# Performance work log

Measured on AMD Instinct MI355X. Metric: run time of the kernel, lower is better.

## Reference

```python
import jax, jax.numpy as jnp
import numpy as np

B, T, D = 64, 512, 512
H, DH = 8, 64  # head_num, att_embedding_size; H*DH == D
NEG = jnp.float32(-2.0**32 + 1)


def _pos_encoding(t, d):
    # Position_Embedding (mode='sum'): [cos, sin] concat over d/2 frequencies
    inv_freq = 1.0 / jnp.power(10000.0, 2.0 * jnp.arange(d // 2, dtype=jnp.float32) / d)
    pij = jnp.arange(t, dtype=jnp.float32)[:, None] * inv_freq[None, :]  # (T, d/2)
    return jnp.concatenate([jnp.cos(pij), jnp.sin(pij)], axis=-1)  # (T, d)


def setup_inputs() -> dict:
    key = jax.random.key(0)
    ks = jax.random.split(key, 9)
    queries = jax.random.normal(ks[0], (B, T, D), dtype=jnp.float32)
    keys = jax.random.normal(ks[1], (B, T, D), dtype=jnp.float32)
    query_lens = jax.random.randint(ks[2], (B, 1), 1, T + 1)
    key_lens = jax.random.randint(ks[3], (B, 1), 1, T + 1)
    W_Q = jax.random.truncated_normal(ks[4], -2., 2., (D, H * DH), dtype=jnp.float32) * 0.05
    W_K = jax.random.truncated_normal(ks[5], -2., 2., (D, H * DH), dtype=jnp.float32) * 0.05
    W_V = jax.random.truncated_normal(ks[6], -2., 2., (D, H * DH), dtype=jnp.float32) * 0.05
    fw1 = jax.random.normal(ks[7], (H * DH, 4 * H * DH), dtype=jnp.float32) * 0.02
    fw2 = jax.random.normal(ks[8], (4 * H * DH, H * DH), dtype=jnp.float32) * 0.02
    return {"queries": queries, "keys": keys, "query_lens": query_lens,
            "key_lens": key_lens, "W_Q": W_Q, "W_K": W_K, "W_V": W_V,
            "fw1": fw1, "fw2": fw2}


def reference(queries, keys, query_lens, key_lens, W_Q, W_K, W_V, fw1, fw2):
    # sequence masks (B, T) from lengths (B, 1)
    ar = jnp.arange(T)
    q_mask = (ar[None, :] < query_lens).astype(jnp.float32)  # (B, T)
    k_mask = ar[None, :] < key_lens                          # (B, T) bool

    pe = _pos_encoding(T, D)[None]  # (1, T, D)
    q_in = queries + pe
    k_in = keys + pe

    qp = jnp.einsum('btd,de->bte', q_in, W_Q).reshape(B, T, H, DH)
    kp = jnp.einsum('btd,de->bte', k_in, W_K)
    # DeepCTR quirk: values projected from the already-projected keys
    vp = jnp.einsum('btd,de->bte', kp, W_V).reshape(B, T, H, DH)
    kp = kp.reshape(B, T, H, DH)

    scores = jnp.einsum('bthd,bshd->bhts', qp, kp) / jnp.sqrt(jnp.float32(DH))
    scores = jnp.where(k_mask[:, None, None, :], scores, NEG)
    scores = scores - jnp.max(scores, axis=-1, keepdims=True)
    attn = jax.nn.softmax(scores, axis=-1)
    attn = attn * q_mask[:, None, :, None]

    out = jnp.einsum('bhts,bshd->bthd', attn, vp).reshape(B, T, H * DH)
    result = out + q_in  # residual uses PE-augmented queries

    ff = jnp.einsum('btd,df->btf', jax.nn.relu(jnp.einsum('btd,df->btf', result, fw1)), fw2)
    result = result + ff

    return jnp.mean(result, axis=1, keepdims=True)  # (B, 1, D)
```

## Files before the change

kernel.cpp:

```cpp
#include <hip/hip_runtime.h>

typedef unsigned short u16;
typedef __attribute__((ext_vector_type(8))) short short8;
typedef __attribute__((ext_vector_type(4))) float floatx4;

#define LOG2E 1.44269504f

__device__ __forceinline__ u16 f2bf(float x) {
  union { float f; unsigned u; } un; un.f = x;
  unsigned r = un.u + 0x7fffu + ((un.u >> 16) & 1u);
  return (u16)(r >> 16);
}
__device__ __forceinline__ float bf2f(u16 h) {
  union { unsigned u; float f; } un; un.u = ((unsigned)h) << 16;
  return un.f;
}
__device__ __forceinline__ void gld16(const u16* g, u16* l) {
  __builtin_amdgcn_global_load_lds((__attribute__((address_space(1))) void*)g,
                                   (__attribute__((address_space(3))) void*)l, 16, 0, 0);
}

__global__ __launch_bounds__(256) void wtrans_kernel(const float* __restrict__ in,
                                                     u16* __restrict__ out, int K, int N) {
  __shared__ float tile[32][33];
  int tx = threadIdx.x, ty = threadIdx.y;
  int n0 = blockIdx.x * 32, k0 = blockIdx.y * 32;
#pragma unroll
  for (int i = 0; i < 4; i++) {
    int kk = ty + i * 8;
    tile[kk][tx] = in[(size_t)(k0 + kk) * N + n0 + tx];
  }
  __syncthreads();
#pragma unroll
  for (int i = 0; i < 4; i++) {
    int nn = ty + i * 8;
    out[(size_t)(n0 + nn) * K + k0 + tx] = f2bf(tile[tx][nn]);
  }
}

__global__ __launch_bounds__(256) void pe_add_kernel(const float* __restrict__ q,
                                                     const float* __restrict__ k,
                                                     u16* __restrict__ qb, u16* __restrict__ kb) {
  size_t flat = ((size_t)blockIdx.x * 256 + threadIdx.x) * 4;
  int d0 = (int)(flat & 511);
  int t = (int)((flat >> 9) & 511);
  const float4 qv = *(const float4*)(q + flat);
  const float4 kv = *(const float4*)(k + flat);
  float pe[4];
#pragma unroll
  for (int i = 0; i < 4; i++) {
    int d = d0 + i;
    int j = (d < 256) ? d : d - 256;
    float f = exp2f((float)j * -0.05190512648f);
    float arg = (float)t * f;
    pe[i] = (d < 256) ? cosf(arg) : sinf(arg);
  }
  u16 qo[4], ko[4];
  qo[0] = f2bf(qv.x + pe[0]); qo[1] = f2bf(qv.y + pe[1]);
  qo[2] = f2bf(qv.z + pe[2]); qo[3] = f2bf(qv.w + pe[3]);
  ko[0] = f2bf(kv.x + pe[0]); ko[1] = f2bf(kv.y + pe[1]);
  ko[2] = f2bf(kv.z + pe[2]); ko[3] = f2bf(kv.w + pe[3]);
  *(uint2*)(qb + flat) = *(const uint2*)qo;
  *(uint2*)(kb + flat) = *(const uint2*)ko;
}

template <int EPI, int DUAL>
__global__ __launch_bounds__(256) void gemm_bt(const u16* __restrict__ A, const u16* __restrict__ Bt,
                                               u16* __restrict__ C, int NX, int KS, int N, int K,
                                               float* __restrict__ outp,
                                               const u16* __restrict__ A2, const u16* __restrict__ Bt2,
                                               u16* __restrict__ C2) {
  __shared__ u16 Alds[128 * 64];
  __shared__ u16 Blds[128 * 64];
  const int tid = threadIdx.x;
  const int lane = tid & 63, w = tid >> 6;
  const int quad = lane >> 4, cl = lane & 15;
  const int wm = w >> 1, wn = w & 1;
  int L = blockIdx.x;
  if (DUAL) {
    int half = gridDim.x >> 1;
    if (L >= half) { L -= half; A = A2; Bt = Bt2; C = C2; }
  }
  const int xcd = L & 7, s = L >> 3;
  const int nx = s % NX;
  const int t2 = s / NX;
  const int ksl = t2 % KS;
  const int rgrp = t2 / KS;
  const int tm = (rgrp * 8 + xcd) * 128;
  const int tn = nx * 128;
  const int kbase = ksl * (K / KS);
  floatx4 acc[4][4] = {};
  const int nk = (K / KS) >> 6;
  const int srow = lane >> 3;
  const int sg = (lane & 7) ^ srow;
  for (int ks = 0; ks < nk; ks++) {
    __syncthreads();
    const int k0 = kbase + (ks << 6);
#pragma unroll
    for (int i = 0; i < 4; i++) {
      int c = w * 4 + i;
      int row = c * 8 + srow;
      gld16(A + ((size_t)(tm + row) * K + k0 + sg * 8), &Alds[c * 512]);
      gld16(Bt + ((size_t)(tn + row) * K + k0 + sg * 8), &Blds[c * 512]);
    }
    __syncthreads();
#pragma unroll
    for (int kh = 0; kh < 2; kh++) {
      short8 af[4], bfr[4];
      const int ga = (((kh << 2) + quad) ^ (cl & 7)) * 8;
#pragma unroll
      for (int f = 0; f < 4; f++) {
        af[f] = *(const short8*)&Alds[(wm * 64 + f * 16 + cl) * 64 + ga];
        bfr[f] = *(const short8*)&Blds[(wn * 64 + f * 16 + cl) * 64 + ga];
      }
#pragma unroll
      for (int fm = 0; fm < 4; fm++)
#pragma unroll
        for (int fn = 0; fn < 4; fn++)
          acc[fm][fn] = __builtin_amdgcn_mfma_f32_16x16x32_bf16(af[fm], bfr[fn], acc[fm][fn], 0, 0, 0);
    }
  }
  if constexpr (EPI == 0) {
#pragma unroll
    for (int fm = 0; fm < 4; fm++)
#pragma unroll
      for (int fn = 0; fn < 4; fn++)
#pragma unroll
        for (int r = 0; r < 4; r++) {
          int row = tm + wm * 64 + fm * 16 + quad * 4 + r;
          int col = tn + wn * 64 + fn * 16 + cl;
          C[(size_t)row * N + col] = f2bf(acc[fm][fn][r]);
        }
  } else if constexpr (EPI == 2) {
    __shared__ float red[256];
    float csum[4] = {0.f, 0.f, 0.f, 0.f};
#pragma unroll
    for (int fm = 0; fm < 4; fm++)
#pragma unroll
      for (int fn = 0; fn < 4; fn++)
#pragma unroll
        for (int r = 0; r < 4; r++) csum[fn] += fmaxf(acc[fm][fn][r], 0.0f);
#pragma unroll
    for (int fn = 0; fn < 4; fn++) {
      csum[fn] += __shfl_xor(csum[fn], 16);
      csum[fn] += __shfl_xor(csum[fn], 32);
    }
    __syncthreads();
    if (quad == 0) {
#pragma unroll
      for (int fn = 0; fn < 4; fn++) red[wm * 128 + wn * 64 + fn * 16 + cl] = csum[fn];
    }
    __syncthreads();
    if (tid < 128) {
      int wn2 = tid >> 6, c2 = tid & 63;
      float tot = red[wn2 * 64 + c2] + red[128 + wn2 * 64 + c2];
      int b = tm >> 9;
      atomicAdd(outp + (size_t)b * N + tn + wn2 * 64 + c2, tot);
    }
  } else {
    __shared__ u16 Tr[128][130];
#pragma unroll
    for (int fm = 0; fm < 4; fm++)
#pragma unroll
      for (int fn = 0; fn < 4; fn++)
#pragma unroll
        for (int r = 0; r < 4; r++) {
          int row = wm * 64 + fm * 16 + quad * 4 + r;
          int col = wn * 64 + fn * 16 + cl;
          Tr[col][row] = f2bf(acc[fm][fn][r]);
        }
    __syncthreads();
    int col = tid >> 1, half = tid & 1;
    int b = tm >> 9, gcol = tn + col;
    int h = gcol >> 6, d = gcol & 63;
    int s0 = (tm & 511) + half * 64;
    u16* dst = C + ((size_t)((b * 8 + h) * 64 + d) * 512 + s0);
    const u16* src = &Tr[col][half * 64];
#pragma unroll
    for (int j = 0; j < 8; j++) *(short8*)(dst + j * 8) = *(const short8*)(src + j * 8);
  }
}

__global__ __launch_bounds__(256) void ffn2_mean_kernel(const float* __restrict__ sums,
                                                        const float* __restrict__ fw2,
                                                        float* __restrict__ outp) {
  __shared__ float s[128];
  int fs = blockIdx.x & 15, b = blockIdx.x >> 4;
  int tid = threadIdx.x;
  if (tid < 128) s[tid] = sums[(size_t)b * 2048 + fs * 128 + tid];
  __syncthreads();
  const float* w = fw2 + (size_t)(fs * 128) * 512;
  float a0 = 0.f, a1 = 0.f;
#pragma unroll 4
  for (int f = 0; f < 128; f++) {
    float sv = s[f];
    a0 += sv * w[(size_t)f * 512 + tid];
    a1 += sv * w[(size_t)f * 512 + 256 + tid];
  }
  atomicAdd(outp + b * 512 + tid, a0 * (1.0f / 512.0f));
  atomicAdd(outp + b * 512 + 256 + tid, a1 * (1.0f / 512.0f));
}

__global__ __launch_bounds__(256) void attn_kernel(const u16* __restrict__ qp, const u16* __restrict__ kp,
                                                   const u16* __restrict__ vT, const u16* __restrict__ qin,
                                                   u16* __restrict__ resout, const int* __restrict__ qlen,
                                                   const int* __restrict__ klen, float* __restrict__ outp) {
  __shared__ u16 Klds[128 * 64];
  __shared__ u16 Vlds[64 * 128];
  __shared__ u16 Plds[4][16 * 136];
  __shared__ float Csum[4][64];
  int bid = blockIdx.x;
  int qt = bid & 7, h = (bid >> 3) & 7, b = bid >> 6;
  int tid = threadIdx.x, lane = tid & 63, w = tid >> 6;
  int quad = lane >> 4, cl = lane & 15;
  int kl = klen[b], ql = qlen[b];
  int q0 = qt * 64 + w * 16;

  if (qt * 64 >= ql) {
    int c = tid & 63, r0 = (tid >> 6) * 16;
    float s = 0.f;
#pragma unroll
    for (int i = 0; i < 16; i++) {
      size_t idx = ((size_t)(b * 512 + qt * 64 + r0 + i) * 512) + h * 64 + c;
      u16 val = qin[idx];
      resout[idx] = val;
      s += bf2f(val);
    }
    Csum[w][c] = s;
    __syncthreads();
    if (tid < 64) {
      float t = Csum[0][tid] + Csum[1][tid] + Csum[2][tid] + Csum[3][tid];
      atomicAdd(outp + b * 512 + h * 64 + tid, t * (1.0f / 512.0f));
    }
    return;
  }
  bool wactive = q0 < ql;

  short8 qfrag[2];
#pragma unroll
  for (int ks = 0; ks < 2; ks++)
    qfrag[ks] = *(const short8*)(qp + ((size_t)(b * 512 + q0 + cl) * 512 + h * 64 + ks * 32 + quad * 8));
  float m_r[4], l_r[4];
  floatx4 o[4] = {};
#pragma unroll
  for (int r = 0; r < 4; r++) { m_r[r] = -3.0e38f; l_r[r] = 0.f; }

  int nkt = (kl + 127) >> 7;
  for (int kt = 0; kt < nkt; kt++) {
    __syncthreads();
#pragma unroll
    for (int i = 0; i < 4; i++) {
      int c = w * 4 + i;
      int row = c * 8 + (lane >> 3);
      int gc = (lane & 7) ^ (row & 7);
      gld16(kp + ((size_t)(b * 512 + kt * 128 + row) * 512 + h * 64 + gc * 8), &Klds[c * 512]);
    }
#pragma unroll
    for (int i = 0; i < 4; i++) {
      int c = w * 4 + i;
      int row = c * 4 + (lane >> 4);
      int gc = (lane & 15) ^ (row & 7);
      gld16(vT + ((size_t)((b * 8 + h) * 64 + row) * 512 + kt * 128 + gc * 8), &Vlds[c * 512]);
    }
    __syncthreads();
    if (!wactive) continue;
    floatx4 sacc[8] = {};
#pragma unroll
    for (int f = 0; f < 8; f++) {
      int krow = f * 16 + cl;
#pragma unroll
      for (int ks = 0; ks < 2; ks++) {
        int kc = ks * 4 + quad;
        short8 kf = *(const short8*)&Klds[krow * 64 + ((kc ^ (cl & 7)) * 8)];
        sacc[f] = __builtin_amdgcn_mfma_f32_16x16x32_bf16(qfrag[ks], kf, sacc[f], 0, 0, 0);
      }
    }
    float mnew[4];
#pragma unroll
    for (int r = 0; r < 4; r++) mnew[r] = m_r[r];
#pragma unroll
    for (int f = 0; f < 8; f++) {
      int key = kt * 128 + f * 16 + cl;
      bool ok = key < kl;
#pragma unroll
      for (int r = 0; r < 4; r++) {
        float v = ok ? sacc[f][r] * 0.125f : -4294967296.0f;
        sacc[f][r] = v;
        mnew[r] = fmaxf(mnew[r], v);
      }
    }
#pragma unroll
    for (int mk = 1; mk <= 8; mk <<= 1)
#pragma unroll
      for (int r = 0; r < 4; r++) mnew[r] = fmaxf(mnew[r], __shfl_xor(mnew[r], mk));
    float alpha[4], lad[4];
#pragma unroll
    for (int r = 0; r < 4; r++) {
      alpha[r] = exp2f((m_r[r] - mnew[r]) * LOG2E);
      lad[r] = 0.f;
      m_r[r] = mnew[r];
    }
#pragma unroll
    for (int f = 0; f < 8; f++)
#pragma unroll
      for (int r = 0; r < 4; r++) {
        float p = exp2f((sacc[f][r] - mnew[r]) * LOG2E);
        lad[r] += p;
        Plds[w][(quad * 4 + r) * 136 + f * 16 + cl] = f2bf(p);
      }
#pragma unroll
    for (int mk = 1; mk <= 8; mk <<= 1)
#pragma unroll
      for (int r = 0; r < 4; r++) lad[r] += __shfl_xor(lad[r], mk);
#pragma unroll
    for (int r = 0; r < 4; r++) l_r[r] = l_r[r] * alpha[r] + lad[r];
#pragma unroll
    for (int fd = 0; fd < 4; fd++)
#pragma unroll
      for (int r = 0; r < 4; r++) o[fd][r] *= alpha[r];
#pragma unroll
    for (int k2 = 0; k2 < 4; k2++) {
      short8 pf = *(const short8*)&Plds[w][cl * 136 + k2 * 32 + quad * 8];
#pragma unroll
      for (int fd = 0; fd < 4; fd++) {
        int vrow = fd * 16 + cl;
        int sc = k2 * 4 + quad;
        short8 vf = *(const short8*)&Vlds[vrow * 128 + ((sc ^ (cl & 7)) * 8)];
        o[fd] = __builtin_amdgcn_mfma_f32_16x16x32_bf16(pf, vf, o[fd], 0, 0, 0);
      }
    }
  }
  float colsum[4] = {0.f, 0.f, 0.f, 0.f};
#pragma unroll
  for (int fd = 0; fd < 4; fd++)
#pragma unroll
    for (int r = 0; r < 4; r++) {
      int q = q0 + quad * 4 + r;
      float v = o[fd][r] / l_r[r];
      if (q >= ql) v = 0.f;
      size_t idx = (size_t)(b * 512 + q) * 512 + h * 64 + fd * 16 + cl;
      v += bf2f(qin[idx]);
      resout[idx] = f2bf(v);
      colsum[fd] += v;
    }
#pragma unroll
  for (int fd = 0; fd < 4; fd++) {
    colsum[fd] += __shfl_xor(colsum[fd], 16);
    colsum[fd] += __shfl_xor(colsum[fd], 32);
  }
  if (quad == 0) {
#pragma unroll
    for (int fd = 0; fd < 4; fd++) Csum[w][fd * 16 + cl] = colsum[fd];
  }
  __syncthreads();
  if (tid < 64) {
    float t = Csum[0][tid] + Csum[1][tid] + Csum[2][tid] + Csum[3][tid];
    atomicAdd(outp + b * 512 + h * 64 + tid, t * (1.0f / 512.0f));
  }
}

extern "C" void kernel_launch(void* const* d_in, const int* in_sizes, int n_in,
                              void* d_out, int out_size, void* d_ws, size_t ws_size,
                              hipStream_t stream) {
  const float* queries = (const float*)d_in[0];
  const float* keys = (const float*)d_in[1];
  const int* qlen = (const int*)d_in[2];
  const int* klen = (const int*)d_in[3];
  const float* W_Q = (const float*)d_in[4];
  const float* W_K = (const float*)d_in[5];
  const float* W_V = (const float*)d_in[6];
  const float* fw1 = (const float*)d_in[7];
  const float* fw2 = (const float*)d_in[8];
  float* outp = (float*)d_out;
  char* ws = (char*)d_ws;

  constexpr size_t SZ_W = 512 * 512 * 2;
  constexpr size_t SZ_F = 2048 * 512 * 2;
  constexpr size_t SZ_S = 64 * 2048 * 4;
  constexpr size_t SZ_T = (size_t)64 * 512 * 512 * 2;
  size_t o_WqT = 0;
  size_t o_WkT = o_WqT + SZ_W;
  size_t o_WvT = o_WkT + SZ_W;
  size_t o_F1T = o_WvT + SZ_W;
  size_t o_SUM = o_F1T + SZ_F;
  size_t o_ABCD = o_SUM + SZ_S;
  size_t o_E = o_ABCD + 4 * SZ_T;
  size_t NEED = o_E + SZ_T;
  if (ws_size < NEED) return;

  u16* WqT = (u16*)(ws + o_WqT);
  u16* WkT = (u16*)(ws + o_WkT);
  u16* WvT = (u16*)(ws + o_WvT);
  u16* F1T = (u16*)(ws + o_F1T);
  float* sums = (float*)(ws + o_SUM);
  u16* q_in = (u16*)(ws + o_ABCD);
  u16* k_in = (u16*)(ws + o_ABCD + SZ_T);
  u16* qp = (u16*)(ws + o_ABCD + 2 * SZ_T);
  u16* kpb = (u16*)(ws + o_ABCD + 3 * SZ_T);
  u16* vT = k_in;
  u16* resb = (u16*)(ws + o_E);

  hipMemsetAsync(d_out, 0, (size_t)out_size * sizeof(float), stream);
  hipMemsetAsync(sums, 0, SZ_S, stream);

  dim3 tb(32, 8);
  wtrans_kernel<<<dim3(16, 16), tb, 0, stream>>>(W_Q, WqT, 512, 512);
  wtrans_kernel<<<dim3(16, 16), tb, 0, stream>>>(W_K, WkT, 512, 512);
  wtrans_kernel<<<dim3(16, 16), tb, 0, stream>>>(W_V, WvT, 512, 512);
  wtrans_kernel<<<dim3(64, 16), tb, 0, stream>>>(fw1, F1T, 512, 2048);

  pe_add_kernel<<<16384, 256, 0, stream>>>(queries, keys, q_in, k_in);

  gemm_bt<0, 1><<<2 * 4 * 256, 256, 0, stream>>>(q_in, WqT, qp, 4, 1, 512, 512, nullptr, k_in, WkT, kpb);
  gemm_bt<3, 0><<<4 * 256, 256, 0, stream>>>(kpb, WvT, vT, 4, 1, 512, 512, nullptr, nullptr, nullptr, nullptr);

  attn_kernel<<<4096, 256, 0, stream>>>(qp, kpb, vT, q_in, resb, qlen, klen, outp);

  gemm_bt<2, 0><<<16 * 256, 256, 0, stream>>>(resb, F1T, nullptr, 16, 1, 2048, 512, sums, nullptr, nullptr, nullptr);
  ffn2_mean_kernel<<<1024, 256, 0, stream>>>(sums, fw2, outp);
}
```

Before: 423.9 us.

## Stage full per-head K/V in LDS once and loop all query tiles per block

Measured after the change: 459.4 us. 8.4% more time.

```diff
diff --git a/kernel.cpp b/kernel.cpp
--- a/kernel.cpp
+++ b/kernel.cpp
@@ -205,144 +205,149 @@
                                                    const u16* __restrict__ vT, const u16* __restrict__ qin,
                                                    u16* __restrict__ resout, const int* __restrict__ qlen,
                                                    const int* __restrict__ klen, float* __restrict__ outp) {
-  __shared__ u16 Klds[128 * 64];
-  __shared__ u16 Vlds[64 * 128];
+  __shared__ u16 Klds[4 * 128 * 64];
+  __shared__ u16 Vlds[4 * 64 * 128];
   __shared__ u16 Plds[4][16 * 136];
-  __shared__ float Csum[4][64];
-  int bid = blockIdx.x;
-  int qt = bid & 7, h = (bid >> 3) & 7, b = bid >> 6;
-  int tid = threadIdx.x, lane = tid & 63, w = tid >> 6;
-  int quad = lane >> 4, cl = lane & 15;
-  int kl = klen[b], ql = qlen[b];
-  int q0 = qt * 64 + w * 16;
-
-  if (qt * 64 >= ql) {
-    int c = tid & 63, r0 = (tid >> 6) * 16;
-    float s = 0.f;
-#pragma unroll
-    for (int i = 0; i < 16; i++) {
-      size_t idx = ((size_t)(b * 512 + qt * 64 + r0 + i) * 512) + h * 64 + c;
-      u16 val = qin[idx];
-      resout[idx] = val;
-      s += bf2f(val);
-    }
-    Csum[w][c] = s;
-    __syncthreads();
-    if (tid < 64) {
-      float t = Csum[0][tid] + Csum[1][tid] + Csum[2][tid] + Csum[3][tid];
-      atomicAdd(outp + b * 512 + h * 64 + tid, t * (1.0f / 512.0f));
-    }
-    return;
-  }
-  bool wactive = q0 < ql;
-
-  short8 qfrag[2];
-#pragma unroll
-  for (int ks = 0; ks < 2; ks++)
-    qfrag[ks] = *(const short8*)(qp + ((size_t)(b * 512 + q0 + cl) * 512 + h * 64 + ks * 32 + quad * 8));
-  float m_r[4], l_r[4];
-  floatx4 o[4] = {};
-#pragma unroll
-  for (int r = 0; r < 4; r++) { m_r[r] = -3.0e38f; l_r[r] = 0.f; }
-
-  int nkt = (kl + 127) >> 7;
-  for (int kt = 0; kt < nkt; kt++) {
-    __syncthreads();
-#pragma unroll
-    for (int i = 0; i < 4; i++) {
-      int c = w * 4 + i;
-      int row = c * 8 + (lane >> 3);
-      int gc = (lane & 7) ^ (row & 7);
-      gld16(kp + ((size_t)(b * 512 + kt * 128 + row) * 512 + h * 64 + gc * 8), &Klds[c * 512]);
-    }
-#pragma unroll
-    for (int i = 0; i < 4; i++) {
-      int c = w * 4 + i;
-      int row = c * 4 + (lane >> 4);
+  const int bid = blockIdx.x;
+  const int h = bid & 7, b = bid >> 3;
+  const int tid = threadIdx.x, lane = tid & 63, w = tid >> 6;
+  const int quad = lane >> 4, cl = lane & 15;
+  const int kl = klen[b], ql = qlen[b];
+  const int nkt = (kl + 127) >> 7;
+
+  {
+    const int srow = lane >> 3;
+    const int sg = (lane & 7) ^ srow;
+    for (int c = w; c < nkt * 16; c += 4) {
+      int row = (c >> 4) * 128 + (c & 15) * 8 + srow;
+      gld16(kp + ((size_t)(b * 512 + row) * 512 + h * 64 + sg * 8), &Klds[c * 512]);
+    }
+    const int vr = lane >> 4;
+    for (int c = w; c < nkt * 16; c += 4) {
+      int row = (c & 15) * 4 + vr;
       int gc = (lane & 15) ^ (row & 7);
-      gld16(vT + ((size_t)((b * 8 + h) * 64 + row) * 512 + kt * 128 + gc * 8), &Vlds[c * 512]);
-    }
-    __syncthreads();
-    if (!wactive) continue;
-    floatx4 sacc[8] = {};
-#pragma unroll
-    for (int f = 0; f < 8; f++) {
-      int krow = f * 16 + cl;
-#pragma unroll
-      for (int ks = 0; ks < 2; ks++) {
-        int kc = ks * 4 + quad;
-        short8 kf = *(const short8*)&Klds[krow * 64 + ((kc ^ (cl & 7)) * 8)];
-        sacc[f] = __builtin_amdgcn_mfma_f32_16x16x32_bf16(qfrag[ks], kf, sacc[f], 0, 0, 0);
-      }
-    }
-    float mnew[4];
-#pragma unroll
-    for (int r = 0; r < 4; r++) mnew[r] = m_r[r];
-#pragma unroll
-    for (int f = 0; f < 8; f++) {
-      int key = kt * 128 + f * 16 + cl;
-      bool ok = key < kl;
+      gld16(vT + ((size_t)((b * 8 + h) * 64 + row) * 512 + (c >> 4) * 128 + gc * 8), &Vlds[c * 512]);
+    }
+  }
+
+  float colsum[4] = {0.f, 0.f, 0.f, 0.f};
+
+#pragma unroll 1
+  for (int p = 0; p < 8; p++) {
+    int q0 = p * 64 + w * 16;
+    if (q0 < ql) continue;
+#pragma unroll
+    for (int fd = 0; fd < 4; fd++)
 #pragma unroll
       for (int r = 0; r < 4; r++) {
-        float v = ok ? sacc[f][r] * 0.125f : -4294967296.0f;
-        sacc[f][r] = v;
-        mnew[r] = fmaxf(mnew[r], v);
-      }
-    }
-#pragma unroll
-    for (int mk = 1; mk <= 8; mk <<= 1)
-#pragma unroll
-      for (int r = 0; r < 4; r++) mnew[r] = fmaxf(mnew[r], __shfl_xor(mnew[r], mk));
-    float alpha[4], lad[4];
-#pragma unroll
-    for (int r = 0; r < 4; r++) {
-      alpha[r] = exp2f((m_r[r] - mnew[r]) * LOG2E);
-      lad[r] = 0.f;
-      m_r[r] = mnew[r];
-    }
-#pragma unroll
-    for (int f = 0; f < 8; f++)
+        int q = q0 + quad * 4 + r;
+        size_t idx = ((size_t)(b * 512 + q) * 512) + h * 64 + fd * 16 + cl;
+        u16 val = qin[idx];
+        resout[idx] = val;
+        colsum[fd] += bf2f(val);
+      }
+  }
+
+  __syncthreads();
+
+#pragma unroll 1
+  for (int p = 0; p < 8; p++) {
+    int q0 = p * 64 + w * 16;
+    if (q0 >= ql) continue;
+    short8 qfrag[2];
+#pragma unroll
+    for (int ks = 0; ks < 2; ks++)
+      qfrag[ks] = *(const short8*)(qp + ((size_t)(b * 512 + q0 + cl) * 512 + h * 64 + ks * 32 + quad * 8));
+    float m_r[4], l_r[4];
+    floatx4 o[4] = {};
+#pragma unroll
+    for (int r = 0; r < 4; r++) { m_r[r] = -3.0e38f; l_r[r] = 0.f; }
+
+#pragma unroll 1
+    for (int kt = 0; kt < nkt; kt++) {
+      const u16* Kt = &Klds[kt * 8192];
+      const u16* Vt = &Vlds[kt * 8192];
+      floatx4 sacc[8] = {};
+#pragma unroll
+      for (int f = 0; f < 8; f++) {
+        int krow = f * 16 + cl;
+#pragma unroll
+        for (int ks = 0; ks < 2; ks++) {
+          int kc = ks * 4 + quad;
+          short8 kf = *(const short8*)&Kt[krow * 64 + ((kc ^ (cl & 7)) * 8)];
+          sacc[f] = __builtin_amdgcn_mfma_f32_16x16x32_bf16(qfrag[ks], kf, sacc[f], 0, 0, 0);
+        }
+      }
+      float mnew[4];
+#pragma unroll
+      for (int r = 0; r < 4; r++) mnew[r] = m_r[r];
+#pragma unroll
+      for (int f = 0; f < 8; f++) {
+        int key = kt * 128 + f * 16 + cl;
+        bool ok = key < kl;
+#pragma unroll
+        for (int r = 0; r < 4; r++) {
+          float v = ok ? sacc[f][r] * 0.125f : -4294967296.0f;
+          sacc[f][r] = v;
+          mnew[r] = fmaxf(mnew[r], v);
+        }
+      }
+#pragma unroll
+      for (int mk = 1; mk <= 8; mk <<= 1)
+#pragma unroll
+        for (int r = 0; r < 4; r++) mnew[r] = fmaxf(mnew[r], __shfl_xor(mnew[r], mk));
+      float alpha[4], lad[4];
 #pragma unroll
       for (int r = 0; r < 4; r++) {
-        float p = exp2f((sacc[f][r] - mnew[r]) * LOG2E);
-        lad[r] += p;
-        Plds[w][(quad * 4 + r) * 136 + f * 16 + cl] = f2bf(p);
-      }
-#pragma unroll
-    for (int mk = 1; mk <= 8; mk <<= 1)
-#pragma unroll
-      for (int r = 0; r < 4; r++) lad[r] += __shfl_xor(lad[r], mk);
-#pragma unroll
-    for (int r = 0; r < 4; r++) l_r[r] = l_r[r] * alpha[r] + lad[r];
+        alpha[r] = exp2f((m_r[r] - mnew[r]) * LOG2E);
+        lad[r] = 0.f;
+        m_r[r] = mnew[r];
+      }
+#pragma unroll
+      for (int f = 0; f < 8; f++)
+#pragma unroll
+        for (int r = 0; r < 4; r++) {
+          float pv = exp2f((sacc[f][r] - mnew[r]) * LOG2E);
+          lad[r] += pv;
+          Plds[w][(quad * 4 + r) * 136 + f * 16 + cl] = f2bf(pv);
+        }
+#pragma unroll
+      for (int mk = 1; mk <= 8; mk <<= 1)
+#pragma unroll
+        for (int r = 0; r < 4; r++) lad[r] += __shfl_xor(lad[r], mk);
+#pragma unroll
+      for (int r = 0; r < 4; r++) l_r[r] = l_r[r] * alpha[r] + lad[r];
+#pragma unroll
+      for (int fd = 0; fd < 4; fd++)
+#pragma unroll
+        for (int r = 0; r < 4; r++) o[fd][r] *= alpha[r];
+#pragma unroll
+      for (int k2 = 0; k2 < 4; k2++) {
+        short8 pf = *(const short8*)&Plds[w][cl * 136 + k2 * 32 + quad * 8];
+#pragma unroll
+        for (int fd = 0; fd < 4; fd++) {
+          int vrow = fd * 16 + cl;
+          int sc = k2 * 4 + quad;
+          short8 vf = *(const short8*)&Vt[vrow * 128 + ((sc ^ (cl & 7)) * 8)];
+          o[fd] = __builtin_amdgcn_mfma_f32_16x16x32_bf16(pf, vf, o[fd], 0, 0, 0);
+        }
+      }
+    }
+
 #pragma unroll
     for (int fd = 0; fd < 4; fd++)
 #pragma unroll
-      for (int r = 0; r < 4; r++) o[fd][r] *= alpha[r];
-#pragma unroll
-    for (int k2 = 0; k2 < 4; k2++) {
-      short8 pf = *(const short8*)&Plds[w][cl * 136 + k2 * 32 + quad * 8];
-#pragma unroll
-      for (int fd = 0; fd < 4; fd++) {
-        int vrow = fd * 16 + cl;
-        int sc = k2 * 4 + quad;
-        short8 vf = *(const short8*)&Vlds[vrow * 128 + ((sc ^ (cl & 7)) * 8)];
-        o[fd] = __builtin_amdgcn_mfma_f32_16x16x32_bf16(pf, vf, o[fd], 0, 0, 0);
-      }
-    }
-  }
-  float colsum[4] = {0.f, 0.f, 0.f, 0.f};
-#pragma unroll
-  for (int fd = 0; fd < 4; fd++)
-#pragma unroll
-    for (int r = 0; r < 4; r++) {
-      int q = q0 + quad * 4 + r;
-      float v = o[fd][r] / l_r[r];
-      if (q >= ql) v = 0.f;
-      size_t idx = (size_t)(b * 512 + q) * 512 + h * 64 + fd * 16 + cl;
-      v += bf2f(qin[idx]);
-      resout[idx] = f2bf(v);
-      colsum[fd] += v;
-    }
+      for (int r = 0; r < 4; r++) {
+        int q = q0 + quad * 4 + r;
+        float v = o[fd][r] / l_r[r];
+        if (q >= ql) v = 0.f;
+        size_t idx = (size_t)(b * 512 + q) * 512 + h * 64 + fd * 16 + cl;
+        v += bf2f(qin[idx]);
+        resout[idx] = f2bf(v);
+        colsum[fd] += v;
+      }
+  }
+
 #pragma unroll
   for (int fd = 0; fd < 4; fd++) {
     colsum[fd] += __shfl_xor(colsum[fd], 16);
@@ -350,12 +355,8 @@
   }
   if (quad == 0) {
 #pragma unroll
-    for (int fd = 0; fd < 4; fd++) Csum[w][fd * 16 + cl] = colsum[fd];
-  }
-  __syncthreads();
-  if (tid < 64) {
-    float t = Csum[0][tid] + Csum[1][tid] + Csum[2][tid] + Csum[3][tid];
-    atomicAdd(outp + b * 512 + h * 64 + tid, t * (1.0f / 512.0f));
+    for (int fd = 0; fd < 4; fd++)
+      atomicAdd(outp + b * 512 + h * 64 + fd * 16 + cl, colsum[fd] * (1.0f / 512.0f));
   }
 }
 
@@ -414,7 +415,7 @@
   gemm_bt<0, 1><<<2 * 4 * 256, 256, 0, stream>>>(q_in, WqT, qp, 4, 1, 512, 512, nullptr, k_in, WkT, kpb);
   gemm_bt<3, 0><<<4 * 256, 256, 0, stream>>>(kpb, WvT, vT, 4, 1, 512, 512, nullptr, nullptr, nullptr, nullptr);
 
-  attn_kernel<<<4096, 256, 0, stream>>>(qp, kpb, vT, q_in, resb, qlen, klen, outp);
+  attn_kernel<<<64 * 8, 256, 0, stream>>>(qp, kpb, vT, q_in, resb, qlen, klen, outp);
 
   gemm_bt<2, 0><<<16 * 256, 256, 0, stream>>>(resb, F1T, nullptr, 16, 1, 2048, 512, sums, nullptr, nullptr, nullptr);
   ffn2_mean_kernel<<<1024, 256, 0, stream>>>(sums, fw2, outp);
```

## Alias P buffer onto K tile in LDS and remap blocks across XCDs

Applied to the files above, without the earlier changes.

New measurement: 416.3 us. No clear change (-1.8%).

```diff
diff --git a/kernel.cpp b/kernel.cpp
--- a/kernel.cpp
+++ b/kernel.cpp
@@ -205,12 +205,15 @@
                                                    const u16* __restrict__ vT, const u16* __restrict__ qin,
                                                    u16* __restrict__ resout, const int* __restrict__ qlen,
                                                    const int* __restrict__ klen, float* __restrict__ outp) {
-  __shared__ u16 Klds[128 * 64];
+  __shared__ u16 KPu[8704];
   __shared__ u16 Vlds[64 * 128];
-  __shared__ u16 Plds[4][16 * 136];
   __shared__ float Csum[4][64];
-  int bid = blockIdx.x;
-  int qt = bid & 7, h = (bid >> 3) & 7, b = bid >> 6;
+  int L = blockIdx.x;
+  int xcd = L & 7;
+  int idx = L >> 3;
+  int qt = idx & 7;
+  int g = xcd + (idx >> 3) * 8;
+  int h = g & 7, b = g >> 3;
   int tid = threadIdx.x, lane = tid & 63, w = tid >> 6;
   int quad = lane >> 4, cl = lane & 15;
   int kl = klen[b], ql = qlen[b];
@@ -221,9 +224,9 @@
     float s = 0.f;
 #pragma unroll
     for (int i = 0; i < 16; i++) {
-      size_t idx = ((size_t)(b * 512 + qt * 64 + r0 + i) * 512) + h * 64 + c;
-      u16 val = qin[idx];
-      resout[idx] = val;
+      size_t idx2 = ((size_t)(b * 512 + qt * 64 + r0 + i) * 512) + h * 64 + c;
+      u16 val = qin[idx2];
+      resout[idx2] = val;
       s += bf2f(val);
     }
     Csum[w][c] = s;
@@ -253,7 +256,7 @@
       int c = w * 4 + i;
       int row = c * 8 + (lane >> 3);
       int gc = (lane & 7) ^ (row & 7);
-      gld16(kp + ((size_t)(b * 512 + kt * 128 + row) * 512 + h * 64 + gc * 8), &Klds[c * 512]);
+      gld16(kp + ((size_t)(b * 512 + kt * 128 + row) * 512 + h * 64 + gc * 8), &KPu[c * 512]);
     }
 #pragma unroll
     for (int i = 0; i < 4; i++) {
@@ -263,70 +266,74 @@
       gld16(vT + ((size_t)((b * 8 + h) * 64 + row) * 512 + kt * 128 + gc * 8), &Vlds[c * 512]);
     }
     __syncthreads();
-    if (!wactive) continue;
     floatx4 sacc[8] = {};
-#pragma unroll
-    for (int f = 0; f < 8; f++) {
-      int krow = f * 16 + cl;
-#pragma unroll
-      for (int ks = 0; ks < 2; ks++) {
-        int kc = ks * 4 + quad;
-        short8 kf = *(const short8*)&Klds[krow * 64 + ((kc ^ (cl & 7)) * 8)];
-        sacc[f] = __builtin_amdgcn_mfma_f32_16x16x32_bf16(qfrag[ks], kf, sacc[f], 0, 0, 0);
+    float mnew[4], alpha[4];
+    if (wactive) {
+#pragma unroll
+      for (int f = 0; f < 8; f++) {
+        int krow = f * 16 + cl;
+#pragma unroll
+        for (int ks = 0; ks < 2; ks++) {
+          int kc = ks * 4 + quad;
+          short8 kf = *(const short8*)&KPu[krow * 64 + ((kc ^ (cl & 7)) * 8)];
+          sacc[f] = __builtin_amdgcn_mfma_f32_16x16x32_bf16(qfrag[ks], kf, sacc[f], 0, 0, 0);
+        }
       }
-    }
-    float mnew[4];
-#pragma unroll
-    for (int r = 0; r < 4; r++) mnew[r] = m_r[r];
-#pragma unroll
-    for (int f = 0; f < 8; f++) {
-      int key = kt * 128 + f * 16 + cl;
-      bool ok = key < kl;
+#pragma unroll
+      for (int r = 0; r < 4; r++) mnew[r] = m_r[r];
+#pragma unroll
+      for (int f = 0; f < 8; f++) {
+        int key = kt * 128 + f * 16 + cl;
+        bool ok = key < kl;
+#pragma unroll
+        for (int r = 0; r < 4; r++) {
+          float v = ok ? sacc[f][r] * 0.125f : -4294967296.0f;
+          sacc[f][r] = v;
+          mnew[r] = fmaxf(mnew[r], v);
+        }
+      }
+#pragma unroll
+      for (int mk = 1; mk <= 8; mk <<= 1)
+#pragma unroll
+        for (int r = 0; r < 4; r++) mnew[r] = fmaxf(mnew[r], __shfl_xor(mnew[r], mk));
 #pragma unroll
       for (int r = 0; r < 4; r++) {
-        float v = ok ? sacc[f][r] * 0.125f : -4294967296.0f;
-        sacc[f][r] = v;
-        mnew[r] = fmaxf(mnew[r], v);
+        alpha[r] = exp2f((m_r[r] - mnew[r]) * LOG2E);
+        m_r[r] = mnew[r];
       }
     }
-#pragma unroll
-    for (int mk = 1; mk <= 8; mk <<= 1)
-#pragma unroll
-      for (int r = 0; r < 4; r++) mnew[r] = fmaxf(mnew[r], __shfl_xor(mnew[r], mk));
-    float alpha[4], lad[4];
-#pragma unroll
-    for (int r = 0; r < 4; r++) {
-      alpha[r] = exp2f((m_r[r] - mnew[r]) * LOG2E);
-      lad[r] = 0.f;
-      m_r[r] = mnew[r];
-    }
-#pragma unroll
-    for (int f = 0; f < 8; f++)
-#pragma unroll
-      for (int r = 0; r < 4; r++) {
-        float p = exp2f((sacc[f][r] - mnew[r]) * LOG2E);
-        lad[r] += p;
-        Plds[w][(quad * 4 + r) * 136 + f * 16 + cl] = f2bf(p);
-      }
-#pragma unroll
-    for (int mk = 1; mk <= 8; mk <<= 1)
-#pragma unroll
-      for (int r = 0; r < 4; r++) lad[r] += __shfl_xor(lad[r], mk);
-#pragma unroll
-    for (int r = 0; r < 4; r++) l_r[r] = l_r[r] * alpha[r] + lad[r];
-#pragma unroll
-    for (int fd = 0; fd < 4; fd++)
-#pragma unroll
-      for (int r = 0; r < 4; r++) o[fd][r] *= alpha[r];
-#pragma unroll
-    for (int k2 = 0; k2 < 4; k2++) {
-      short8 pf = *(const short8*)&Plds[w][cl * 136 + k2 * 32 + quad * 8];
-#pragma unroll
-      for (int fd = 0; fd < 4; fd++) {
-        int vrow = fd * 16 + cl;
-        int sc = k2 * 4 + quad;
-        short8 vf = *(const short8*)&Vlds[vrow * 128 + ((sc ^ (cl & 7)) * 8)];
-        o[fd] = __builtin_amdgcn_mfma_f32_16x16x32_bf16(pf, vf, o[fd], 0, 0, 0);
+    __syncthreads();
+    if (wactive) {
+      u16* P = &KPu[w * 2176];
+      float lad[4] = {0.f, 0.f, 0.f, 0.f};
+#pragma unroll
+      for (int f = 0; f < 8; f++)
+#pragma unroll
+        for (int r = 0; r < 4; r++) {
+          float p = exp2f((sacc[f][r] - mnew[r]) * LOG2E);
+          lad[r] += p;
+          P[(quad * 4 + r) * 136 + f * 16 + cl] = f2bf(p);
+        }
+#pragma unroll
+      for (int mk = 1; mk <= 8; mk <<= 1)
+#pragma unroll
+        for (int r = 0; r < 4; r++) lad[r] += __shfl_xor(lad[r], mk);
+#pragma unroll
+      for (int r = 0; r < 4; r++) l_r[r] = l_r[r] * alpha[r] + lad[r];
+#pragma unroll
+      for (int fd = 0; fd < 4; fd++)
+#pragma unroll
+        for (int r = 0; r < 4; r++) o[fd][r] *= alpha[r];
+#pragma unroll
+      for (int k2 = 0; k2 < 4; k2++) {
+        short8 pf = *(const short8*)&P[cl * 136 + k2 * 32 + quad * 8];
+#pragma unroll
+        for (int fd = 0; fd < 4; fd++) {
+          int vrow = fd * 16 + cl;
+          int sc = k2 * 4 + quad;
+          short8 vf = *(const short8*)&Vlds[vrow * 128 + ((sc ^ (cl & 7)) * 8)];
+          o[fd] = __builtin_amdgcn_mfma_f32_16x16x32_bf16(pf, vf, o[fd], 0, 0, 0);
+        }
       }
     }
   }
@@ -338,9 +345,9 @@
       int q = q0 + quad * 4 + r;
       float v = o[fd][r] / l_r[r];
       if (q >= ql) v = 0.f;
-      size_t idx = (size_t)(b * 512 + q) * 512 + h * 64 + fd * 16 + cl;
-      v += bf2f(qin[idx]);
-      resout[idx] = f2bf(v);
+      size_t idx2 = (size_t)(b * 512 + q) * 512 + h * 64 + fd * 16 + cl;
+      v += bf2f(qin[idx2]);
+      resout[idx2] = f2bf(v);
       colsum[fd] += v;
     }
 #pragma unroll
```
